# Kernel optimization log

Hardware: AMD Instinct MI355X
Metric: run time of the kernel (lower is better)

## Reference

```python
import math
import jax, jax.numpy as jnp
import numpy as np

IN_DIM, OUT_DIM, NUM_BASIS = 128, 64, 8
EPS = 1e-5

def _periods():
    # periods[i,j,g] = i*(out_dim*num_basis) + j*num_basis + g + 2
    i = jnp.arange(OUT_DIM)[:, None, None]
    j = jnp.arange(OUT_DIM)[None, :, None]
    g = jnp.arange(NUM_BASIS)[None, None, :]
    return (i * (OUT_DIM * NUM_BASIS) + j * NUM_BASIS + g + 2).astype(jnp.float32)

def setup_inputs() -> dict:
    key = jax.random.key(0)
    k1, k2, k3, k4 = jax.random.split(key, 4)
    x = jax.random.normal(k1, (2, 512, IN_DIM), dtype=jnp.float32)
    positions = jnp.arange(512, dtype=jnp.int32)
    M = jax.random.uniform(k2, (OUT_DIM, IN_DIM), minval=-0.5, maxval=0.5, dtype=jnp.float32)
    P = jax.random.uniform(k3, (OUT_DIM, OUT_DIM, NUM_BASIS), minval=-0.1, maxval=0.1, dtype=jnp.float32)
    gamma = jnp.ones((OUT_DIM,), dtype=jnp.float32)
    beta = jnp.zeros((OUT_DIM,), dtype=jnp.float32)
    Wres = jax.random.uniform(k4, (OUT_DIM, IN_DIM), minval=-0.1, maxval=0.1, dtype=jnp.float32)
    return {"x": x, "positions": positions, "M": M, "P": P, "gamma": gamma, "beta": beta, "Wres": Wres}

def reference(x, positions, M, P, gamma, beta, Wres):
    # x: (b, s, in), M: (out, in)
    x_trans = jnp.einsum('bsc,oc->bso', x, M)
    mu = jnp.mean(x_trans, axis=-1, keepdims=True)
    var = jnp.mean(jnp.square(x_trans - mu), axis=-1, keepdims=True)
    x_trans = (x_trans - mu) * jax.lax.rsqrt(var + EPS) * gamma + beta
    # phi[s,i,j,g] = cos(2*pi*k_s / periods[i,j,g])
    k = positions.astype(jnp.float32)[:, None, None, None]
    phi = jnp.cos(2.0 * math.pi * k / _periods())  # (s, out, out, nb)
    # Nk[b,s,i] = sum_{j,g} P[i,j,g] * x_trans[b,s,j] * phi[s,i,j,g]
    W = jnp.einsum('sijg,ijg->sij', phi, P)  # (s, out, out)
    Nk = jnp.einsum('bsj,sij->bsi', x_trans, W)
    residual = jnp.einsum('bsc,oc->bso', x, Wres)  # separate residual proj (in!=out)
    return Nk + residual
```

## Files before the change

### kernel.cpp

```cpp
#include <hip/hip_runtime.h>
#include <hip/hip_bf16.h>

#define IN_DIM    128
#define OUT_DIM   64
#define NUM_BASIS 8
#define SEQ       512
#define BATCH     2
#define EPS       1e-5f
#define SX        2

__global__ __launch_bounds__(512) void fused_layerts_kernel(
    const float* __restrict__ x,
    const float* __restrict__ M,
    const float* __restrict__ Wres,
    const float* __restrict__ gamma,
    const float* __restrict__ beta,
    const float* __restrict__ P,
    const int*   __restrict__ positions,
    float* __restrict__ out)
{
    const int s0  = blockIdx.x * SX;
    const int tid = threadIdx.x;

    __shared__ float xs [SX][BATCH][IN_DIM];
    __shared__ float xts[SX][BATCH][OUT_DIM];
    __shared__ float rs [SX][BATCH][OUT_DIM];
    __shared__ float pm [2][SX * BATCH][OUT_DIM];
    __shared__ float pr [2][SX * BATCH][OUT_DIM];
    __shared__ float part[8][SX][BATCH][OUT_DIM];

    {
        const int row = tid >> 7;
        const int c   = tid & 127;
        const int b   = row & 1;
        const int sl  = row >> 1;
        xs[sl][b][c] = x[((size_t)b * SEQ + (s0 + sl)) * IN_DIM + c];
    }
    const float k0 = (float)positions[s0];
    const float k1 = (float)positions[s0 + 1];
    __syncthreads();

    {
        const int o    = tid & 63;
        const int r    = (tid >> 6) & 3;
        const int half = tid >> 8;
        const int b    = r & 1;
        const int sl   = r >> 1;

        const float4* x4 = reinterpret_cast<const float4*>(&xs[sl][b][half * 64]);
        const float4* m4 = reinterpret_cast<const float4*>(M    + (size_t)o * IN_DIM + half * 64);
        const float4* w4 = reinterpret_cast<const float4*>(Wres + (size_t)o * IN_DIM + half * 64);

        float macc = 0.f, racc = 0.f;
#pragma unroll
        for (int c = 0; c < 16; ++c) {
            float4 xv = x4[c];
            float4 mv = m4[c];
            float4 wv = w4[c];
            macc += xv.x * mv.x + xv.y * mv.y + xv.z * mv.z + xv.w * mv.w;
            racc += xv.x * wv.x + xv.y * wv.y + xv.z * wv.z + xv.w * wv.w;
        }
        pm[half][r][o] = macc;
        pr[half][r][o] = racc;
    }
    __syncthreads();

    if (tid < SX * BATCH * OUT_DIM) {
        const int o  = tid & 63;
        const int r  = tid >> 6;
        const int b  = r & 1;
        const int sl = r >> 1;

        const float macc = pm[0][r][o] + pm[1][r][o];
        const float racc = pr[0][r][o] + pr[1][r][o];

        float ssum = macc;
#pragma unroll
        for (int off = 32; off > 0; off >>= 1) ssum += __shfl_xor(ssum, off);
        const float mu = ssum * (1.0f / OUT_DIM);

        const float d = macc - mu;
        float v = d * d;
#pragma unroll
        for (int off = 32; off > 0; off >>= 1) v += __shfl_xor(v, off);
        const float var = v * (1.0f / OUT_DIM);

        xts[sl][b][o] = d * rsqrtf(var + EPS) * gamma[o] + beta[o];
        rs [sl][b][o] = racc;
    }
    __syncthreads();

    const int i   = tid & 63;
    const int grp = tid >> 6;

    float nk00 = 0.f, nk01 = 0.f, nk10 = 0.f, nk11 = 0.f;

#pragma unroll
    for (int jj = 0; jj < 8; ++jj) {
        const int j    = grp * 8 + jj;
        const int base = (i * OUT_DIM + j) * NUM_BASIS;
        const float4* Pp = reinterpret_cast<const float4*>(P + base);
        const float4 p0 = Pp[0];
        const float4 p1 = Pp[1];
        const float basef = (float)(base + 2);

        const float pv[8] = {p0.x, p0.y, p0.z, p0.w, p1.x, p1.y, p1.z, p1.w};
        float w0 = 0.f, w1 = 0.f;
#pragma unroll
        for (int g = 0; g < NUM_BASIS; ++g) {
            const float period = basef + (float)g;
            const float inv = __builtin_amdgcn_rcpf(period);
            float t0 = __builtin_amdgcn_fractf(k0 * inv);
            float t1 = __builtin_amdgcn_fractf(k1 * inv);
            w0 += pv[g] * __builtin_amdgcn_cosf(t0);
            w1 += pv[g] * __builtin_amdgcn_cosf(t1);
        }
        nk00 += xts[0][0][j] * w0;
        nk01 += xts[0][1][j] * w0;
        nk10 += xts[1][0][j] * w1;
        nk11 += xts[1][1][j] * w1;
    }

    part[grp][0][0][i] = nk00;
    part[grp][0][1][i] = nk01;
    part[grp][1][0][i] = nk10;
    part[grp][1][1][i] = nk11;
    __syncthreads();

    if (tid < SX * BATCH * OUT_DIM) {
        const int o  = tid & 63;
        const int r  = tid >> 6;
        const int b  = r & 1;
        const int sl = r >> 1;

        float sum = 0.f;
#pragma unroll
        for (int gg = 0; gg < 8; ++gg) sum += part[gg][sl][b][o];

        const size_t idx = ((size_t)b * SEQ + (s0 + sl)) * OUT_DIM + o;
        out[idx] = sum + rs[sl][b][o];
    }
}

extern "C" void kernel_launch(void* const* d_in, const int* in_sizes, int n_in,
                              void* d_out, int out_size, void* d_ws, size_t ws_size,
                              hipStream_t stream)
{
    const float* x         = (const float*)d_in[0];
    const int*   positions = (const int*)d_in[1];
    const float* M         = (const float*)d_in[2];
    const float* P         = (const float*)d_in[3];
    const float* gamma     = (const float*)d_in[4];
    const float* beta      = (const float*)d_in[5];
    const float* Wres      = (const float*)d_in[6];
    float* out = (float*)d_out;

    hipLaunchKernelGGL(fused_layerts_kernel, dim3(SEQ / SX), dim3(512), 0, stream,
                       x, M, Wres, gamma, beta, P, positions, out);
}
```

Measured before the change: 18.48 us.

## Interleave basis-weight computation with projections and read x directly from global

The basis-weighted cosine sums (w0/w1) now run before the layernorm barrier and are interleaved with the M/Wres projection dot products, so transcendental work can overlap global-memory latency. The shared-memory staging of x and its barrier are removed, and each thread reads x straight from global memory. Sixteen weight values are held in registers across the barriers, which raises register pressure, and the x rows are now loaded redundantly by many threads.

```diff
diff --git a/kernel.cpp b/kernel.cpp
--- a/kernel.cpp
+++ b/kernel.cpp
@@ -21,124 +21,117 @@
 {
     const int s0  = blockIdx.x * SX;
     const int tid = threadIdx.x;
+    const int o   = tid & 63;
+    const int rq  = tid >> 6;
+    const int r   = rq & 3;
+    const int half= rq >> 2;
+    const int b   = r & 1;
+    const int sl  = r >> 1;
 
-    __shared__ float xs [SX][BATCH][IN_DIM];
+    __shared__ float pm [2][SX * BATCH][OUT_DIM];
+    __shared__ float pr [2][SX * BATCH][OUT_DIM];
     __shared__ float xts[SX][BATCH][OUT_DIM];
     __shared__ float rs [SX][BATCH][OUT_DIM];
-    __shared__ float pm [2][SX * BATCH][OUT_DIM];
-    __shared__ float pr [2][SX * BATCH][OUT_DIM];
     __shared__ float part[8][SX][BATCH][OUT_DIM];
 
-    {
-        const int row = tid >> 7;
-        const int c   = tid & 127;
-        const int b   = row & 1;
-        const int sl  = row >> 1;
-        xs[sl][b][c] = x[((size_t)b * SEQ + (s0 + sl)) * IN_DIM + c];
-    }
     const float k0 = (float)positions[s0];
     const float k1 = (float)positions[s0 + 1];
-    __syncthreads();
 
-    {
-        const int o    = tid & 63;
-        const int r    = (tid >> 6) & 3;
-        const int half = tid >> 8;
-        const int b    = r & 1;
-        const int sl   = r >> 1;
+    const float4* x4 = reinterpret_cast<const float4*>(
+        x + ((size_t)b * SEQ + (s0 + sl)) * IN_DIM + half * 64);
+    const float4* m4 = reinterpret_cast<const float4*>(
+        M + (size_t)o * IN_DIM + half * 64);
+    const float4* w4 = reinterpret_cast<const float4*>(
+        Wres + (size_t)o * IN_DIM + half * 64);
 
-        const float4* x4 = reinterpret_cast<const float4*>(&xs[sl][b][half * 64]);
-        const float4* m4 = reinterpret_cast<const float4*>(M    + (size_t)o * IN_DIM + half * 64);
-        const float4* w4 = reinterpret_cast<const float4*>(Wres + (size_t)o * IN_DIM + half * 64);
+    float w0[8], w1[8];
+    float macc = 0.f, racc = 0.f;
 
-        float macc = 0.f, racc = 0.f;
 #pragma unroll
-        for (int c = 0; c < 16; ++c) {
+    for (int jj = 0; jj < 8; ++jj) {
+        const int j    = rq * 8 + jj;
+        const int base = (o * OUT_DIM + j) * NUM_BASIS;
+        const float4* Pp = reinterpret_cast<const float4*>(P + base);
+        const float4 p0 = Pp[0];
+        const float4 p1 = Pp[1];
+        const float basef = (float)(base + 2);
+
+        const float pv[8] = {p0.x, p0.y, p0.z, p0.w, p1.x, p1.y, p1.z, p1.w};
+        float a0 = 0.f, a1 = 0.f;
+#pragma unroll
+        for (int g = 0; g < NUM_BASIS; ++g) {
+            const float inv = __builtin_amdgcn_rcpf(basef + (float)g);
+            a0 += pv[g] * __builtin_amdgcn_cosf(__builtin_amdgcn_fractf(k0 * inv));
+            a1 += pv[g] * __builtin_amdgcn_cosf(__builtin_amdgcn_fractf(k1 * inv));
+        }
+        w0[jj] = a0;
+        w1[jj] = a1;
+
+#pragma unroll
+        for (int cc = 0; cc < 2; ++cc) {
+            const int c = jj * 2 + cc;
             float4 xv = x4[c];
             float4 mv = m4[c];
             float4 wv = w4[c];
             macc += xv.x * mv.x + xv.y * mv.y + xv.z * mv.z + xv.w * mv.w;
             racc += xv.x * wv.x + xv.y * wv.y + xv.z * wv.z + xv.w * wv.w;
         }
-        pm[half][r][o] = macc;
-        pr[half][r][o] = racc;
     }
+
+    pm[half][r][o] = macc;
+    pr[half][r][o] = racc;
     __syncthreads();
 
     if (tid < SX * BATCH * OUT_DIM) {
-        const int o  = tid & 63;
-        const int r  = tid >> 6;
-        const int b  = r & 1;
-        const int sl = r >> 1;
+        const int r2  = tid >> 6;
+        const int b2  = r2 & 1;
+        const int sl2 = r2 >> 1;
 
-        const float macc = pm[0][r][o] + pm[1][r][o];
-        const float racc = pr[0][r][o] + pr[1][r][o];
+        const float m2  = pm[0][r2][o] + pm[1][r2][o];
+        const float rr2 = pr[0][r2][o] + pr[1][r2][o];
 
-        float ssum = macc;
+        float ssum = m2;
 #pragma unroll
         for (int off = 32; off > 0; off >>= 1) ssum += __shfl_xor(ssum, off);
         const float mu = ssum * (1.0f / OUT_DIM);
 
-        const float d = macc - mu;
+        const float d = m2 - mu;
         float v = d * d;
 #pragma unroll
         for (int off = 32; off > 0; off >>= 1) v += __shfl_xor(v, off);
         const float var = v * (1.0f / OUT_DIM);
 
-        xts[sl][b][o] = d * rsqrtf(var + EPS) * gamma[o] + beta[o];
-        rs [sl][b][o] = racc;
+        xts[sl2][b2][o] = d * rsqrtf(var + EPS) * gamma[o] + beta[o];
+        rs [sl2][b2][o] = rr2;
     }
     __syncthreads();
 
-    const int i   = tid & 63;
-    const int grp = tid >> 6;
-
     float nk00 = 0.f, nk01 = 0.f, nk10 = 0.f, nk11 = 0.f;
-
 #pragma unroll
     for (int jj = 0; jj < 8; ++jj) {
-        const int j    = grp * 8 + jj;
-        const int base = (i * OUT_DIM + j) * NUM_BASIS;
-        const float4* Pp = reinterpret_cast<const float4*>(P + base);
-        const float4 p0 = Pp[0];
-        const float4 p1 = Pp[1];
-        const float basef = (float)(base + 2);
-
-        const float pv[8] = {p0.x, p0.y, p0.z, p0.w, p1.x, p1.y, p1.z, p1.w};
-        float w0 = 0.f, w1 = 0.f;
-#pragma unroll
-        for (int g = 0; g < NUM_BASIS; ++g) {
-            const float period = basef + (float)g;
-            const float inv = __builtin_amdgcn_rcpf(period);
-            float t0 = __builtin_amdgcn_fractf(k0 * inv);
-            float t1 = __builtin_amdgcn_fractf(k1 * inv);
-            w0 += pv[g] * __builtin_amdgcn_cosf(t0);
-            w1 += pv[g] * __builtin_amdgcn_cosf(t1);
-        }
-        nk00 += xts[0][0][j] * w0;
-        nk01 += xts[0][1][j] * w0;
-        nk10 += xts[1][0][j] * w1;
-        nk11 += xts[1][1][j] * w1;
+        const int j = rq * 8 + jj;
+        nk00 += xts[0][0][j] * w0[jj];
+        nk01 += xts[0][1][j] * w0[jj];
+        nk10 += xts[1][0][j] * w1[jj];
+        nk11 += xts[1][1][j] * w1[jj];
     }
-
-    part[grp][0][0][i] = nk00;
-    part[grp][0][1][i] = nk01;
-    part[grp][1][0][i] = nk10;
-    part[grp][1][1][i] = nk11;
+    part[rq][0][0][o] = nk00;
+    part[rq][0][1][o] = nk01;
+    part[rq][1][0][o] = nk10;
+    part[rq][1][1][o] = nk11;
     __syncthreads();
 
     if (tid < SX * BATCH * OUT_DIM) {
-        const int o  = tid & 63;
-        const int r  = tid >> 6;
-        const int b  = r & 1;
-        const int sl = r >> 1;
+        const int r2  = tid >> 6;
+        const int b2  = r2 & 1;
+        const int sl2 = r2 >> 1;
 
         float sum = 0.f;
 #pragma unroll
-        for (int gg = 0; gg < 8; ++gg) sum += part[gg][sl][b][o];
+        for (int gg = 0; gg < 8; ++gg) sum += part[gg][sl2][b2][o];
 
-        const size_t idx = ((size_t)b * SEQ + (s0 + sl)) * OUT_DIM + o;
-        out[idx] = sum + rs[sl][b][o];
+        const size_t idx = ((size_t)b2 * SEQ + (s0 + sl2)) * OUT_DIM + o;
+        out[idx] = sum + rs[sl2][b2][o];
     }
 }
 
```

New measurement: 19.47 us. 5.4% more time.
